# Optimization experiments

Measured on AMD Instinct MI355X. Metric: run time of the kernel, lower is better.

Reference implementation:

```python
import jax, jax.numpy as jnp
import numpy as np

B, S, E, H = 8, 2048, 512, 8
HD = E // H
N_IND = 64


def setup_inputs() -> dict:
    key = jax.random.key(0)
    ks = jax.random.split(key, 10)
    s = 1.0 / np.sqrt(E)
    return {
        "x": jax.random.normal(ks[0], (B, S, E), jnp.float32),
        "Wq": jax.random.normal(ks[1], (E, E), jnp.float32) * s,
        "bq": jax.random.normal(ks[2], (E,), jnp.float32) * s,
        "Wk": jax.random.normal(ks[3], (E, E), jnp.float32) * s,
        "bk": jax.random.normal(ks[4], (E,), jnp.float32) * s,
        "Wv": jax.random.normal(ks[5], (E, E), jnp.float32) * s,
        "bv": jax.random.normal(ks[6], (E,), jnp.float32) * s,
        "Wo": jax.random.normal(ks[7], (E, E), jnp.float32) * s,
        "bo": jax.random.normal(ks[8], (E,), jnp.float32) * s,
        "industry_ids": jax.random.randint(ks[9], (S,), 0, N_IND, jnp.int32),
    }


def reference(x, Wq, bq, Wk, bk, Wv, bv, Wo, bo, industry_ids):
    # same-industry block mask [S, S]; every row attends at least to itself
    mask = industry_ids[:, None] == industry_ids[None, :]
    # projections (torch Linear: y = x @ W.T + b)
    q = (x @ Wq.T + bq).reshape(B, S, H, HD).transpose(0, 2, 1, 3)  # [B,H,S,HD]
    k = (x @ Wk.T + bk).reshape(B, S, H, HD).transpose(0, 2, 1, 3)
    v = (x @ Wv.T + bv).reshape(B, S, H, HD).transpose(0, 2, 1, 3)
    scores = jnp.einsum("bhqd,bhkd->bhqk", q, k) / np.sqrt(HD).astype(jnp.float32)
    scores = jnp.where(mask[None, None, :, :], scores, -jnp.inf)
    attn = jax.nn.softmax(scores, axis=-1)  # dropout is identity at inference
    out = jnp.einsum("bhqk,bhkd->bhqd", attn, v)
    out = out.transpose(0, 2, 1, 3).reshape(B, S, E)
    return out @ Wo.T + bo
```

## Files before the change

kernel.cpp:

```cpp
#include <hip/hip_runtime.h>
#include <cstdint>

#define DEVFN __device__ __forceinline__

typedef __bf16 bf16x8 __attribute__((ext_vector_type(8)));
typedef float f32x4 __attribute__((ext_vector_type(4)));
typedef unsigned int uint;

constexpr int Bc = 8, Sc = 2048, Ec = 512, Hc = 8, HDc = 64, NI = 64;
constexpr int Mtot = Bc * Sc;
constexpr int Kdim = Ec;
constexpr int MAXITEMS = 128;

DEVFN unsigned short f2bf(float f) {
  unsigned u = __builtin_bit_cast(unsigned, f);
  u += 0x7fffu + ((u >> 16) & 1u);
  return (unsigned short)(u >> 16);
}

typedef const void __attribute__((address_space(1))) gvoid_t;
typedef void __attribute__((address_space(3))) lvoid_t;
DEVFN void gload16(const void* g, void* l) {
  __builtin_amdgcn_global_load_lds((gvoid_t*)g, (lvoid_t*)l, 16, 0, 0);
}

DEVFN uint cvtpk(float lo, float hi) {
  uint r;
  asm("v_cvt_pk_bf16_f32 %0, %1, %2" : "=v"(r) : "v"(lo), "v"(hi));
  return r;
}

#define WAIT_VM_BARRIER(N)                                            \
  do {                                                                \
    asm volatile("s_waitcnt vmcnt(" #N ")\n\ts_barrier" ::: "memory"); \
    __builtin_amdgcn_sched_barrier(0);                                \
  } while (0)
#define WAIT_LGKM_BARRIER()                                            \
  do {                                                                 \
    asm volatile("s_waitcnt lgkmcnt(0)\n\ts_barrier" ::: "memory");    \
    __builtin_amdgcn_sched_barrier(0);                                 \
  } while (0)

__global__ void prep2_kernel(const int* __restrict__ ids, int* __restrict__ perm,
                             int* __restrict__ gstart, int* __restrict__ gsz,
                             int* __restrict__ items, int* __restrict__ nitems,
                             const float* __restrict__ Wq, const float* __restrict__ Wk,
                             const float* __restrict__ Wv, const float* __restrict__ Wo,
                             ushort* __restrict__ Wcat, ushort* __restrict__ Wob,
                             const float* __restrict__ x, ushort* __restrict__ xb) {
  if (blockIdx.x == 0) {
    __shared__ int sid[Sc];
    __shared__ int hist[NI];
    __shared__ int base[NI];
    int t = threadIdx.x;
    if (t < NI) hist[t] = 0;
    for (int i = t; i < Sc; i += 256) sid[i] = ids[i];
    __syncthreads();
    for (int i = t; i < Sc; i += 256) atomicAdd(&hist[sid[i]], 1);
    __syncthreads();
    if (t == 0) {
      int run = 0;
      for (int g = 0; g < NI; ++g) { base[g] = run; run += hist[g]; }
      int cnt = 0;
      for (int g = 0; g < NI; ++g)
        for (int q0 = 0; q0 < hist[g]; q0 += 32) items[cnt++] = (g << 16) | q0;
      *nitems = cnt;
    }
    __syncthreads();
    if (t < NI) { gstart[t] = base[t]; gsz[t] = hist[t]; }
    int lane = t & 63, w = t >> 6;
    for (int g = w; g < NI; g += 4) {
      int run = base[g];
      for (int c = 0; c < Sc; c += 64) {
        int tok = c + lane;
        int id = sid[tok];
        unsigned long long mask = __ballot(id == g);
        if (id == g) {
          int rank = __popcll(mask & ((1ull << lane) - 1ull));
          perm[run + rank] = tok;
        }
        run += __popcll(mask);
      }
    }
  } else if (blockIdx.x <= 1024) {
    int i = (blockIdx.x - 1) * 256 + threadIdx.x;
    int idx = i * 4;
    int n = idx >> 9, k = idx & 511;
    const float* src;
    ushort* dst;
    if (n < 512)       { src = Wq + (size_t)n * 512 + k;          dst = Wcat + (size_t)n * 512 + k; }
    else if (n < 1024) { src = Wk + (size_t)(n - 512) * 512 + k;  dst = Wcat + (size_t)n * 512 + k; }
    else if (n < 1536) { src = Wv + (size_t)(n - 1024) * 512 + k; dst = Wcat + (size_t)n * 512 + k; }
    else               { src = Wo + (size_t)(n - 1536) * 512 + k; dst = Wob + (size_t)(n - 1536) * 512 + k; }
    float4 v = *(const float4*)src;
    ushort4 o = {f2bf(v.x), f2bf(v.y), f2bf(v.z), f2bf(v.w)};
    *(ushort4*)dst = o;
  } else {
    int i = (blockIdx.x - 1025) * 256 + threadIdx.x;
    float4 v = ((const float4*)x)[i];
    ushort4 o = {f2bf(v.x), f2bf(v.y), f2bf(v.z), f2bf(v.w)};
    ((ushort4*)xb)[i] = o;
  }
}

__global__ __launch_bounds__(256) void gemm_qkv128(
    const ushort* __restrict__ A, const ushort* __restrict__ Bw,
    const float* __restrict__ bias0, const float* __restrict__ bias1,
    const float* __restrict__ bias2, const int* __restrict__ permarg,
    ushort* __restrict__ qkvout) {
  constexpr int NK = Kdim / 64;
  __shared__ __align__(16) char ldsraw[65536];
  ushort* sAb = (ushort*)ldsraw;
  ushort* sBb = (ushort*)(ldsraw + 32768);
  const int tid = threadIdx.x;
  const int lane = tid & 63;
  const int wave = tid >> 6;
  const int wr = wave >> 1, wc = wave & 1;
  const int orig = blockIdx.x;
  const int xcd = orig & 7, gl = orig >> 3;
  const int mbase = (xcd * 16 + (gl & 15)) * 128;
  const int nbase = (gl >> 4) * 128;

  f32x4 acc[4][4] = {};

  const int rowS = wave * 32 + (lane >> 3);
  const int kc = lane & 7;
  const int mb_hi = mbase & ~(Sc - 1);

  int arow[4];
#pragma unroll
  for (int c = 0; c < 4; ++c)
    arow[c] = mb_hi | permarg[(mbase + rowS + c * 8) & (Sc - 1)];

  auto stage = [&](int buf, int kt) {
    const int k0 = kt * 64;
#pragma unroll
    for (int c = 0; c < 4; ++c) {
      int row = rowS + c * 8;
      int kcp = (kc ^ (row & 7)) * 8;
      gload16(A + (size_t)arow[c] * Kdim + k0 + kcp,
              sAb + buf * 8192 + (wave * 256 + c * 64) * 8);
      gload16(Bw + (size_t)(nbase + row) * Kdim + k0 + kcp,
              sBb + buf * 8192 + (wave * 256 + c * 64) * 8);
    }
  };

  stage(0, 0);
  stage(1, 1);

  for (int kt = 0; kt < NK; ++kt) {
    const int cur = kt & 1;
    if (kt < NK - 1) {
      WAIT_VM_BARRIER(8);
    } else {
      WAIT_VM_BARRIER(0);
    }

    const char* Ab = (const char*)(sAb + cur * 8192);
    const char* Bb = (const char*)(sBb + cur * 8192);
    __builtin_amdgcn_s_setprio(1);
#pragma unroll
    for (int kk = 0; kk < 2; ++kk) {
      bf16x8 af[4], bfv[4];
#pragma unroll
      for (int i = 0; i < 4; ++i) {
        int row = wr * 64 + i * 16 + (lane & 15);
        int off = row * 128 + kk * 64 + (lane >> 4) * 16;
        off ^= (row & 7) << 4;
        af[i] = *(const bf16x8*)(Ab + off);
      }
#pragma unroll
      for (int j = 0; j < 4; ++j) {
        int col = wc * 64 + j * 16 + (lane & 15);
        int off = col * 128 + kk * 64 + (lane >> 4) * 16;
        off ^= (col & 7) << 4;
        bfv[j] = *(const bf16x8*)(Bb + off);
      }
#pragma unroll
      for (int i = 0; i < 4; ++i)
#pragma unroll
        for (int j = 0; j < 4; ++j)
          acc[i][j] = __builtin_amdgcn_mfma_f32_16x16x32_bf16(af[i], bfv[j], acc[i][j], 0, 0, 0);
    }
    __builtin_amdgcn_s_setprio(0);

    WAIT_LGKM_BARRIER();
    if (kt + 2 < NK) stage(cur, kt + 2);
  }

  {
    ushort* T = (ushort*)ldsraw;
#pragma unroll
    for (int i = 0; i < 4; ++i) {
#pragma unroll
      for (int j = 0; j < 4; ++j) {
        int nl = wc * 64 + j * 16 + (lane & 15);
        int n = nbase + nl;
        float bv = (n < 512) ? bias0[n] : (n < 1024) ? bias1[n - 512] : bias2[n - 1024];
#pragma unroll
        for (int r = 0; r < 4; ++r) {
          int ml = wr * 64 + i * 16 + (lane >> 4) * 4 + r;
          T[ml * 136 + nl] = f2bf(acc[i][j][r] + bv);
        }
      }
    }
    __syncthreads();
#pragma unroll
    for (int k = 0; k < 8; ++k) {
      int c = tid + 256 * k;
      int row = c >> 4, col8 = (c & 15) * 8;
      uint4 w = *(const uint4*)(T + row * 136 + col8);
      int n0 = nbase + col8;
      int proj = n0 >> 9, h = (n0 >> 6) & 7, d0 = n0 & 63;
      int p = mbase + row;
      int bidx = p >> 11, pl = p & (Sc - 1);
      size_t off = (size_t)proj * ((size_t)Bc * Hc * Sc * HDc) +
                   (size_t)((bidx * Hc + h) * Sc + pl) * HDc + d0;
      *(uint4*)(qkvout + off) = w;
    }
  }
}

__global__ __launch_bounds__(256) void gemm_out128(
    const ushort* __restrict__ A, const ushort* __restrict__ Bw,
    const float* __restrict__ bias0, const int* __restrict__ permarg,
    float* __restrict__ out) {
  constexpr int NK = Kdim / 64;
  constexpr int NTOT = 512;
  __shared__ __align__(16) char ldsraw[65536];
  ushort* sAb = (ushort*)ldsraw;
  ushort* sBb = (ushort*)(ldsraw + 32768);
  const int tid = threadIdx.x;
  const int lane = tid & 63;
  const int wave = tid >> 6;
  const int wr = wave >> 1, wc = wave & 1;
  const int orig = blockIdx.x;
  const int xcd = orig & 7, gl = orig >> 3;
  const int mbase = (xcd * 16 + (gl & 15)) * 128;
  const int nbase = (gl >> 4) * 128;

  f32x4 acc[4][4] = {};

  const int rowS = wave * 32 + (lane >> 3);
  const int kc = lane & 7;

  auto stage = [&](int buf, int kt) {
    const int k0 = kt * 64;
#pragma unroll
    for (int c = 0; c < 4; ++c) {
      int row = rowS + c * 8;
      int kcp = (kc ^ (row & 7)) * 8;
      gload16(A + (size_t)(mbase + row) * Kdim + k0 + kcp,
              sAb + buf * 8192 + (wave * 256 + c * 64) * 8);
      gload16(Bw + (size_t)(nbase + row) * Kdim + k0 + kcp,
              sBb + buf * 8192 + (wave * 256 + c * 64) * 8);
    }
  };

  stage(0, 0);
  stage(1, 1);

  for (int kt = 0; kt < NK; ++kt) {
    const int cur = kt & 1;
    if (kt < NK - 1) {
      WAIT_VM_BARRIER(8);
    } else {
      WAIT_VM_BARRIER(0);
    }

    const char* Ab = (const char*)(sAb + cur * 8192);
    const char* Bb = (const char*)(sBb + cur * 8192);
    __builtin_amdgcn_s_setprio(1);
#pragma unroll
    for (int kk = 0; kk < 2; ++kk) {
      bf16x8 af[4], bfv[4];
#pragma unroll
      for (int i = 0; i < 4; ++i) {
        int row = wr * 64 + i * 16 + (lane & 15);
        int off = row * 128 + kk * 64 + (lane >> 4) * 16;
        off ^= (row & 7) << 4;
        af[i] = *(const bf16x8*)(Ab + off);
      }
#pragma unroll
      for (int j = 0; j < 4; ++j) {
        int col = wc * 64 + j * 16 + (lane & 15);
        int off = col * 128 + kk * 64 + (lane >> 4) * 16;
        off ^= (col & 7) << 4;
        bfv[j] = *(const bf16x8*)(Bb + off);
      }
#pragma unroll
      for (int i = 0; i < 4; ++i)
#pragma unroll
        for (int j = 0; j < 4; ++j)
          acc[i][j] = __builtin_amdgcn_mfma_f32_16x16x32_bf16(af[i], bfv[j], acc[i][j], 0, 0, 0);
    }
    __builtin_amdgcn_s_setprio(0);

    WAIT_LGKM_BARRIER();
    if (kt + 2 < NK) stage(cur, kt + 2);
  }

  float* T = (float*)ldsraw;
#pragma unroll
  for (int i = 0; i < 4; ++i) {
#pragma unroll
    for (int j = 0; j < 4; ++j) {
      int nl = wc * 64 + j * 16 + (lane & 15);
      float bv = bias0[nbase + nl];
#pragma unroll
      for (int r = 0; r < 4; ++r) {
        int ml = wr * 64 + i * 16 + (lane >> 4) * 4 + r;
        T[ml * 128 + nl] = acc[i][j][r] + bv;
      }
    }
  }
  __syncthreads();
#pragma unroll
  for (int k = 0; k < 16; ++k) {
    int c = tid + 256 * k;
    int row = c >> 5, col4 = (c & 31) * 4;
    float4 w = *(const float4*)(T + row * 128 + col4);
    int p = mbase + row;
    int bidx = p >> 11;
    int orow = (bidx << 11) | permarg[p & (Sc - 1)];
    *(float4*)(out + (size_t)orow * NTOT + nbase + col4) = w;
  }
}

__global__ __launch_bounds__(64) void attn5_kernel(
    const ushort* __restrict__ qkv, const int* __restrict__ gstart,
    const int* __restrict__ gsz, const int* __restrict__ items,
    const int* __restrict__ nitems, ushort* __restrict__ obuf) {
  __shared__ __align__(16) ushort vt[64 * 40];
  if ((int)blockIdx.x >= *nitems) return;
  const int iv = items[blockIdx.x];
  const int g = iv >> 16, q0 = iv & 0xffff;
  const int bh = blockIdx.y;
  const int start = gstart[g], n = gsz[g];
  const int lane = threadIdx.x;
  const int ql = lane & 15, lg = lane >> 4;

  const size_t planeSz = (size_t)Bc * Hc * Sc * HDc;
  const ushort* qb = qkv + (size_t)bh * Sc * HDc;
  const ushort* kb = qb + planeSz;
  const ushort* vb = kb + planeSz;

  bf16x8 qf[2][2];
#pragma unroll
  for (int qt = 0; qt < 2; ++qt) {
    int row = min(start + q0 + qt * 16 + ql, Sc - 1);
#pragma unroll
    for (int h = 0; h < 2; ++h)
      qf[qt][h] = *(const bf16x8*)(qb + (size_t)row * HDc + h * 32 + lg * 8);
  }

  f32x4 oacc[2][4] = {};
  float lsum[2] = {0.f, 0.f};

  const int vk = lane & 31;
  const int vh = (lane >> 5) * 32;
  const int Lbase = 4 * (ql + 32 * (lg & 1));

  const int npair = (n + 31) >> 5;
  for (int pr = 0; pr < npair; ++pr) {
    const int c0 = pr * 32;
    int vrow = min(start + c0 + vk, Sc - 1);
    const uint4* vp = (const uint4*)(vb + (size_t)vrow * HDc + vh);
    uint4 v0 = vp[0], v1 = vp[1], v2 = vp[2], v3 = vp[3];

    bf16x8 kf[2][2];
#pragma unroll
    for (int t = 0; t < 2; ++t) {
      int row = min(start + c0 + t * 16 + ql, Sc - 1);
#pragma unroll
      for (int h = 0; h < 2; ++h)
        kf[t][h] = *(const bf16x8*)(kb + (size_t)row * HDc + h * 32 + lg * 8);
    }

    uint pw[2][4];
#pragma unroll
    for (int qt = 0; qt < 2; ++qt) {
      f32x4 s0 = {}, s1 = {};
      s0 = __builtin_amdgcn_mfma_f32_16x16x32_bf16(kf[0][0], qf[qt][0], s0, 0, 0, 0);
      s0 = __builtin_amdgcn_mfma_f32_16x16x32_bf16(kf[0][1], qf[qt][1], s0, 0, 0, 0);
      s1 = __builtin_amdgcn_mfma_f32_16x16x32_bf16(kf[1][0], qf[qt][0], s1, 0, 0, 0);
      s1 = __builtin_amdgcn_mfma_f32_16x16x32_bf16(kf[1][1], qf[qt][1], s1, 0, 0, 0);
      float p0[4], p1[4];
      float ls = 0.f;
#pragma unroll
      for (int r = 0; r < 4; ++r) {
        int kk = c0 + 4 * lg + r;
        float e0 = (kk < n) ? __expf(s0[r] * 0.125f) : 0.f;
        float e1 = (kk + 16 < n) ? __expf(s1[r] * 0.125f) : 0.f;
        p0[r] = e0;
        p1[r] = e1;
        ls += e0 + e1;
      }
      lsum[qt] += ls;
      uint a0 = cvtpk(p0[0], p0[1]), b0 = cvtpk(p0[2], p0[3]);
      uint a1 = cvtpk(p1[0], p1[1]), b1 = cvtpk(p1[2], p1[3]);
      uint pA0 = __builtin_amdgcn_ds_bpermute(Lbase, a0);
      uint pB0 = __builtin_amdgcn_ds_bpermute(Lbase, b0);
      uint pA1 = __builtin_amdgcn_ds_bpermute(Lbase, a1);
      uint pB1 = __builtin_amdgcn_ds_bpermute(Lbase, b1);
      uint pC0 = __builtin_amdgcn_ds_bpermute(Lbase + 64, a0);
      uint pD0 = __builtin_amdgcn_ds_bpermute(Lbase + 64, b0);
      uint pC1 = __builtin_amdgcn_ds_bpermute(Lbase + 64, a1);
      uint pD1 = __builtin_amdgcn_ds_bpermute(Lbase + 64, b1);
      bool t0 = lg < 2;
      pw[qt][0] = t0 ? pA0 : pA1;
      pw[qt][1] = t0 ? pB0 : pB1;
      pw[qt][2] = t0 ? pC0 : pC1;
      pw[qt][3] = t0 ? pD0 : pD1;
    }

    {
      uint w[16] = {v0.x, v0.y, v0.z, v0.w, v1.x, v1.y, v1.z, v1.w,
                    v2.x, v2.y, v2.z, v2.w, v3.x, v3.y, v3.z, v3.w};
#pragma unroll
      for (int i = 0; i < 16; ++i) {
        vt[(vh + 2 * i) * 40 + vk] = (ushort)(w[i] & 0xffffu);
        vt[(vh + 2 * i + 1) * 40 + vk] = (ushort)(w[i] >> 16);
      }
    }
    asm volatile("s_waitcnt lgkmcnt(0)" ::: "memory");
    __builtin_amdgcn_sched_barrier(0);
    bf16x8 vf[4];
#pragma unroll
    for (int dq = 0; dq < 4; ++dq)
      vf[dq] = *(const bf16x8*)(vt + (dq * 16 + ql) * 40 + lg * 8);
    asm volatile("s_waitcnt lgkmcnt(0)" ::: "memory");
    __builtin_amdgcn_sched_barrier(0);
#pragma unroll
    for (int qt = 0; qt < 2; ++qt) {
      union { uint u[4]; bf16x8 v; } pf;
      pf.u[0] = pw[qt][0]; pf.u[1] = pw[qt][1]; pf.u[2] = pw[qt][2]; pf.u[3] = pw[qt][3];
#pragma unroll
      for (int dq = 0; dq < 4; ++dq)
        oacc[qt][dq] = __builtin_amdgcn_mfma_f32_16x16x32_bf16(vf[dq], pf.v, oacc[qt][dq], 0, 0, 0);
    }
  }

#pragma unroll
  for (int qt = 0; qt < 2; ++qt) {
    float l = lsum[qt];
    l += __shfl_xor(l, 16);
    l += __shfl_xor(l, 32);
    float inv = 1.f / l;
    int qi = q0 + qt * 16 + ql;
    if (qi < n) {
      int p = start + qi;
      ushort* op = obuf + (size_t)((bh >> 3) * Sc + p) * Ec + (bh & 7) * HDc + lg * 4;
#pragma unroll
      for (int dq = 0; dq < 4; ++dq) {
        uint w0 = cvtpk(oacc[qt][dq][0] * inv, oacc[qt][dq][1] * inv);
        uint w1 = cvtpk(oacc[qt][dq][2] * inv, oacc[qt][dq][3] * inv);
        uint2 wv = {w0, w1};
        *(uint2*)(op + dq * 16) = wv;
      }
    }
  }
}

extern "C" void kernel_launch(void* const* d_in, const int* in_sizes, int n_in,
                              void* d_out, int out_size, void* d_ws, size_t ws_size,
                              hipStream_t stream) {
  const float* x  = (const float*)d_in[0];
  const float* Wq = (const float*)d_in[1];
  const float* bq = (const float*)d_in[2];
  const float* Wk = (const float*)d_in[3];
  const float* bk = (const float*)d_in[4];
  const float* Wv = (const float*)d_in[5];
  const float* bv = (const float*)d_in[6];
  const float* Wo = (const float*)d_in[7];
  const float* bo = (const float*)d_in[8];
  const int* ids  = (const int*)d_in[9];
  float* out = (float*)d_out;

  char* ws = (char*)d_ws;
  ushort* xb   = (ushort*)(ws);
  ushort* Wcat = (ushort*)(ws + 16777216);
  ushort* Wob  = (ushort*)(ws + 18350080);
  ushort* qkv  = (ushort*)(ws + 18874368);
  ushort* obuf = (ushort*)(ws + 69206016);
  int* perm    = (int*)(ws + 85983232);
  int* gstart  = perm + Sc;
  int* gsz     = gstart + NI;
  int* items   = gsz + NI;
  int* nitems  = items + MAXITEMS;

  prep2_kernel<<<dim3(1 + 1024 + Mtot * Ec / 4 / 256), dim3(256), 0, stream>>>(
      ids, perm, gstart, gsz, items, nitems, Wq, Wk, Wv, Wo, Wcat, Wob, x, xb);
  gemm_qkv128<<<dim3(Mtot / 128 * 12), dim3(256), 0, stream>>>(xb, Wcat, bq, bk, bv, perm, qkv);
  attn5_kernel<<<dim3(MAXITEMS, Bc * Hc), dim3(64), 0, stream>>>(qkv, gstart, gsz, items,
                                                                 nitems, obuf);
  gemm_out128<<<dim3(Mtot / 128 * 4), dim3(256), 0, stream>>>(obuf, Wob, bo, perm, out);
}
```

Baseline: 118.4 us.

## Fuse all stages into one persistent kernel with grid-wide barriers

Replaces the four separate launches (prep, QKV GEMM, attention, output GEMM) with one persistent 512-block kernel that loops over work units and separates stages with atomic-counter grid barriers. The goal is to remove launch overhead and inter-kernel drain gaps. In exchange, each stage now runs on a fixed 512-block grid with strided work loops, capped at 2 blocks per CU, and attention runs four waves per block instead of one-wave blocks. The spin barriers require every block to be co-resident, and an extra memset launch is added to reset the counters.

```diff
diff --git a/kernel.cpp b/kernel.cpp
--- a/kernel.cpp
+++ b/kernel.cpp
@@ -11,6 +11,7 @@
 constexpr int Mtot = Bc * Sc;
 constexpr int Kdim = Ec;
 constexpr int MAXITEMS = 128;
+constexpr int NBLK = 512;
 
 DEVFN unsigned short f2bf(float f) {
   unsigned u = __builtin_bit_cast(unsigned, f);
@@ -41,18 +42,38 @@
     __builtin_amdgcn_sched_barrier(0);                                 \
   } while (0)
 
-__global__ void prep2_kernel(const int* __restrict__ ids, int* __restrict__ perm,
-                             int* __restrict__ gstart, int* __restrict__ gsz,
-                             int* __restrict__ items, int* __restrict__ nitems,
-                             const float* __restrict__ Wq, const float* __restrict__ Wk,
-                             const float* __restrict__ Wv, const float* __restrict__ Wo,
-                             ushort* __restrict__ Wcat, ushort* __restrict__ Wob,
-                             const float* __restrict__ x, ushort* __restrict__ xb) {
+DEVFN void grid_bar(int* cnt) {
+  __syncthreads();
+  if (threadIdx.x == 0) {
+    __threadfence();
+    atomicAdd(cnt, 1);
+    while (atomicAdd(cnt, 0) < NBLK) __builtin_amdgcn_s_sleep(2);
+    __threadfence();
+  }
+  __syncthreads();
+}
+
+__global__ __launch_bounds__(256, 2) void mega_kernel(
+    const int* __restrict__ ids, const float* __restrict__ x,
+    const float* __restrict__ Wq, const float* __restrict__ Wk,
+    const float* __restrict__ Wv, const float* __restrict__ Wo,
+    const float* __restrict__ bq, const float* __restrict__ bk,
+    const float* __restrict__ bv, const float* __restrict__ bo,
+    ushort* __restrict__ xb, ushort* __restrict__ Wcat, ushort* __restrict__ Wob,
+    ushort* __restrict__ qkv, ushort* __restrict__ obuf,
+    int* __restrict__ perm, int* __restrict__ gstart, int* __restrict__ gsz,
+    int* __restrict__ items, int* __restrict__ nitems,
+    float* __restrict__ out, int* __restrict__ bars) {
+  __shared__ __align__(16) char ldsraw[65536];
+  const int tid = threadIdx.x;
+  const int lane = tid & 63;
+  const int wave = tid >> 6;
+
   if (blockIdx.x == 0) {
-    __shared__ int sid[Sc];
-    __shared__ int hist[NI];
-    __shared__ int base[NI];
-    int t = threadIdx.x;
+    int* sid = (int*)ldsraw;
+    int* hist = sid + Sc;
+    int* base = hist + NI;
+    int t = tid;
     if (t < NI) hist[t] = 0;
     for (int i = t; i < Sc; i += 256) sid[i] = ids[i];
     __syncthreads();
@@ -68,7 +89,7 @@
     }
     __syncthreads();
     if (t < NI) { gstart[t] = base[t]; gsz[t] = hist[t]; }
-    int lane = t & 63, w = t >> 6;
+    int w = t >> 6;
     for (int g = w; g < NI; g += 4) {
       int run = base[g];
       for (int c = 0; c < Sc; c += 64) {
@@ -82,382 +103,363 @@
         run += __popcll(mask);
       }
     }
-  } else if (blockIdx.x <= 1024) {
-    int i = (blockIdx.x - 1) * 256 + threadIdx.x;
-    int idx = i * 4;
-    int n = idx >> 9, k = idx & 511;
-    const float* src;
-    ushort* dst;
-    if (n < 512)       { src = Wq + (size_t)n * 512 + k;          dst = Wcat + (size_t)n * 512 + k; }
-    else if (n < 1024) { src = Wk + (size_t)(n - 512) * 512 + k;  dst = Wcat + (size_t)n * 512 + k; }
-    else if (n < 1536) { src = Wv + (size_t)(n - 1024) * 512 + k; dst = Wcat + (size_t)n * 512 + k; }
-    else               { src = Wo + (size_t)(n - 1536) * 512 + k; dst = Wob + (size_t)(n - 1536) * 512 + k; }
-    float4 v = *(const float4*)src;
-    ushort4 o = {f2bf(v.x), f2bf(v.y), f2bf(v.z), f2bf(v.w)};
-    *(ushort4*)dst = o;
   } else {
-    int i = (blockIdx.x - 1025) * 256 + threadIdx.x;
-    float4 v = ((const float4*)x)[i];
-    ushort4 o = {f2bf(v.x), f2bf(v.y), f2bf(v.z), f2bf(v.w)};
-    ((ushort4*)xb)[i] = o;
+#pragma unroll 1
+    for (int k = 0; k < 19; ++k) {
+      int unit = (blockIdx.x - 1) + 511 * k;
+      if (unit >= 9216) break;
+      if (unit < 1024) {
+        int i = unit * 256 + tid;
+        int idx = i * 4;
+        int n = idx >> 9, kk = idx & 511;
+        const float* src;
+        ushort* dst;
+        if (n < 512)       { src = Wq + (size_t)n * 512 + kk;          dst = Wcat + (size_t)n * 512 + kk; }
+        else if (n < 1024) { src = Wk + (size_t)(n - 512) * 512 + kk;  dst = Wcat + (size_t)n * 512 + kk; }
+        else if (n < 1536) { src = Wv + (size_t)(n - 1024) * 512 + kk; dst = Wcat + (size_t)n * 512 + kk; }
+        else               { src = Wo + (size_t)(n - 1536) * 512 + kk; dst = Wob + (size_t)(n - 1536) * 512 + kk; }
+        float4 v = *(const float4*)src;
+        ushort4 o = {f2bf(v.x), f2bf(v.y), f2bf(v.z), f2bf(v.w)};
+        *(ushort4*)dst = o;
+      } else {
+        int i = (unit - 1024) * 256 + tid;
+        float4 v = ((const float4*)x)[i];
+        ushort4 o = {f2bf(v.x), f2bf(v.y), f2bf(v.z), f2bf(v.w)};
+        ((ushort4*)xb)[i] = o;
+      }
+    }
   }
-}
-
-__global__ __launch_bounds__(256) void gemm_qkv128(
-    const ushort* __restrict__ A, const ushort* __restrict__ Bw,
-    const float* __restrict__ bias0, const float* __restrict__ bias1,
-    const float* __restrict__ bias2, const int* __restrict__ permarg,
-    ushort* __restrict__ qkvout) {
-  constexpr int NK = Kdim / 64;
-  __shared__ __align__(16) char ldsraw[65536];
-  ushort* sAb = (ushort*)ldsraw;
-  ushort* sBb = (ushort*)(ldsraw + 32768);
-  const int tid = threadIdx.x;
-  const int lane = tid & 63;
-  const int wave = tid >> 6;
-  const int wr = wave >> 1, wc = wave & 1;
-  const int orig = blockIdx.x;
-  const int xcd = orig & 7, gl = orig >> 3;
-  const int mbase = (xcd * 16 + (gl & 15)) * 128;
-  const int nbase = (gl >> 4) * 128;
-
-  f32x4 acc[4][4] = {};
-
-  const int rowS = wave * 32 + (lane >> 3);
-  const int kc = lane & 7;
-  const int mb_hi = mbase & ~(Sc - 1);
-
-  int arow[4];
-#pragma unroll
-  for (int c = 0; c < 4; ++c)
-    arow[c] = mb_hi | permarg[(mbase + rowS + c * 8) & (Sc - 1)];
-
-  auto stage = [&](int buf, int kt) {
-    const int k0 = kt * 64;
-#pragma unroll
-    for (int c = 0; c < 4; ++c) {
-      int row = rowS + c * 8;
-      int kcp = (kc ^ (row & 7)) * 8;
-      gload16(A + (size_t)arow[c] * Kdim + k0 + kcp,
-              sAb + buf * 8192 + (wave * 256 + c * 64) * 8);
-      gload16(Bw + (size_t)(nbase + row) * Kdim + k0 + kcp,
-              sBb + buf * 8192 + (wave * 256 + c * 64) * 8);
-    }
-  };
-
-  stage(0, 0);
-  stage(1, 1);
-
-  for (int kt = 0; kt < NK; ++kt) {
-    const int cur = kt & 1;
-    if (kt < NK - 1) {
-      WAIT_VM_BARRIER(8);
-    } else {
-      WAIT_VM_BARRIER(0);
-    }
-
-    const char* Ab = (const char*)(sAb + cur * 8192);
-    const char* Bb = (const char*)(sBb + cur * 8192);
-    __builtin_amdgcn_s_setprio(1);
-#pragma unroll
-    for (int kk = 0; kk < 2; ++kk) {
-      bf16x8 af[4], bfv[4];
-#pragma unroll
-      for (int i = 0; i < 4; ++i) {
-        int row = wr * 64 + i * 16 + (lane & 15);
-        int off = row * 128 + kk * 64 + (lane >> 4) * 16;
-        off ^= (row & 7) << 4;
-        af[i] = *(const bf16x8*)(Ab + off);
-      }
-#pragma unroll
-      for (int j = 0; j < 4; ++j) {
-        int col = wc * 64 + j * 16 + (lane & 15);
-        int off = col * 128 + kk * 64 + (lane >> 4) * 16;
-        off ^= (col & 7) << 4;
-        bfv[j] = *(const bf16x8*)(Bb + off);
-      }
-#pragma unroll
-      for (int i = 0; i < 4; ++i)
-#pragma unroll
-        for (int j = 0; j < 4; ++j)
-          acc[i][j] = __builtin_amdgcn_mfma_f32_16x16x32_bf16(af[i], bfv[j], acc[i][j], 0, 0, 0);
-    }
-    __builtin_amdgcn_s_setprio(0);
-
-    WAIT_LGKM_BARRIER();
-    if (kt + 2 < NK) stage(cur, kt + 2);
+  grid_bar(&bars[0]);
+
+  {
+    ushort* sAb = (ushort*)ldsraw;
+    ushort* sBb = (ushort*)(ldsraw + 32768);
+    const int wr = wave >> 1, wc = wave & 1;
+    const int rowS = wave * 32 + (lane >> 3);
+    const int kc = lane & 7;
+    constexpr int NK = Kdim / 64;
+#pragma unroll 1
+    for (int t = blockIdx.x; t < 1536; t += NBLK) {
+      const int xcd = t & 7, gl = t >> 3;
+      const int mbase = (xcd * 16 + (gl & 15)) * 128;
+      const int nbase = (gl >> 4) * 128;
+      const int mb_hi = mbase & ~(Sc - 1);
+      f32x4 acc[4][4] = {};
+      int arow[4];
+#pragma unroll
+      for (int c = 0; c < 4; ++c)
+        arow[c] = mb_hi | perm[(mbase + rowS + c * 8) & (Sc - 1)];
+
+      auto stage = [&](int buf, int kt) {
+        const int k0 = kt * 64;
+#pragma unroll
+        for (int c = 0; c < 4; ++c) {
+          int row = rowS + c * 8;
+          int kcp = (kc ^ (row & 7)) * 8;
+          gload16(xb + (size_t)arow[c] * Kdim + k0 + kcp,
+                  sAb + buf * 8192 + (wave * 256 + c * 64) * 8);
+          gload16(Wcat + (size_t)(nbase + row) * Kdim + k0 + kcp,
+                  sBb + buf * 8192 + (wave * 256 + c * 64) * 8);
+        }
+      };
+
+      stage(0, 0);
+      stage(1, 1);
+      for (int kt = 0; kt < NK; ++kt) {
+        const int cur = kt & 1;
+        if (kt < NK - 1) {
+          WAIT_VM_BARRIER(8);
+        } else {
+          WAIT_VM_BARRIER(0);
+        }
+        const char* Ab = (const char*)(sAb + cur * 8192);
+        const char* Bb = (const char*)(sBb + cur * 8192);
+        __builtin_amdgcn_s_setprio(1);
+#pragma unroll
+        for (int kk = 0; kk < 2; ++kk) {
+          bf16x8 af[4], bfv[4];
+#pragma unroll
+          for (int i = 0; i < 4; ++i) {
+            int row = wr * 64 + i * 16 + (lane & 15);
+            int off = row * 128 + kk * 64 + (lane >> 4) * 16;
+            off ^= (row & 7) << 4;
+            af[i] = *(const bf16x8*)(Ab + off);
+          }
+#pragma unroll
+          for (int j = 0; j < 4; ++j) {
+            int col = wc * 64 + j * 16 + (lane & 15);
+            int off = col * 128 + kk * 64 + (lane >> 4) * 16;
+            off ^= (col & 7) << 4;
+            bfv[j] = *(const bf16x8*)(Bb + off);
+          }
+#pragma unroll
+          for (int i = 0; i < 4; ++i)
+#pragma unroll
+            for (int j = 0; j < 4; ++j)
+              acc[i][j] = __builtin_amdgcn_mfma_f32_16x16x32_bf16(af[i], bfv[j], acc[i][j], 0, 0, 0);
+        }
+        __builtin_amdgcn_s_setprio(0);
+        WAIT_LGKM_BARRIER();
+        if (kt + 2 < NK) stage(cur, kt + 2);
+      }
+
+      {
+        ushort* T = (ushort*)ldsraw;
+#pragma unroll
+        for (int i = 0; i < 4; ++i) {
+#pragma unroll
+          for (int j = 0; j < 4; ++j) {
+            int nl = wc * 64 + j * 16 + (lane & 15);
+            int n = nbase + nl;
+            float bvv = (n < 512) ? bq[n] : (n < 1024) ? bk[n - 512] : bv[n - 1024];
+#pragma unroll
+            for (int r = 0; r < 4; ++r) {
+              int ml = wr * 64 + i * 16 + (lane >> 4) * 4 + r;
+              T[ml * 136 + nl] = f2bf(acc[i][j][r] + bvv);
+            }
+          }
+        }
+        __syncthreads();
+#pragma unroll
+        for (int k = 0; k < 8; ++k) {
+          int c = tid + 256 * k;
+          int row = c >> 4, col8 = (c & 15) * 8;
+          uint4 w = *(const uint4*)(T + row * 136 + col8);
+          int n0 = nbase + col8;
+          int proj = n0 >> 9, h = (n0 >> 6) & 7, d0 = n0 & 63;
+          int p = mbase + row;
+          int bidx = p >> 11, pl = p & (Sc - 1);
+          size_t off = (size_t)proj * ((size_t)Bc * Hc * Sc * HDc) +
+                       (size_t)((bidx * Hc + h) * Sc + pl) * HDc + d0;
+          *(uint4*)(qkv + off) = w;
+        }
+      }
+      __syncthreads();
+    }
   }
+  grid_bar(&bars[1]);
 
   {
-    ushort* T = (ushort*)ldsraw;
+    const int NIT = *nitems;
+    ushort* vt = (ushort*)(ldsraw + wave * 5120);
+    const int ql = lane & 15, lg = lane >> 4;
+    const size_t planeSz = (size_t)Bc * Hc * Sc * HDc;
+    const int vk = lane & 31;
+    const int vh = (lane >> 5) * 32;
+    const int Lbase = 4 * (ql + 32 * (lg & 1));
+#pragma unroll 1
+    for (int k = 0; k < 4; ++k) {
+      const int u = (blockIdx.x * 4 + wave) + 2048 * k;
+      const int item = u & (MAXITEMS - 1);
+      const int bh = u >> 7;
+      if (item >= NIT) continue;
+      const int iv = items[item];
+      const int g = iv >> 16, q0 = iv & 0xffff;
+      const int start = gstart[g], n = gsz[g];
+      const ushort* qb = qkv + (size_t)bh * Sc * HDc;
+      const ushort* kb = qb + planeSz;
+      const ushort* vb = kb + planeSz;
+
+      bf16x8 qf[2][2];
+#pragma unroll
+      for (int qt = 0; qt < 2; ++qt) {
+        int row = min(start + q0 + qt * 16 + ql, Sc - 1);
+#pragma unroll
+        for (int h = 0; h < 2; ++h)
+          qf[qt][h] = *(const bf16x8*)(qb + (size_t)row * HDc + h * 32 + lg * 8);
+      }
+      f32x4 oacc[2][4] = {};
+      float lsum[2] = {0.f, 0.f};
+      const int npair = (n + 31) >> 5;
+      for (int pr = 0; pr < npair; ++pr) {
+        const int c0 = pr * 32;
+        int vrow = min(start + c0 + vk, Sc - 1);
+        const uint4* vp = (const uint4*)(vb + (size_t)vrow * HDc + vh);
+        uint4 v0 = vp[0], v1 = vp[1], v2 = vp[2], v3 = vp[3];
+        bf16x8 kf[2][2];
+#pragma unroll
+        for (int t2 = 0; t2 < 2; ++t2) {
+          int row = min(start + c0 + t2 * 16 + ql, Sc - 1);
+#pragma unroll
+          for (int h = 0; h < 2; ++h)
+            kf[t2][h] = *(const bf16x8*)(kb + (size_t)row * HDc + h * 32 + lg * 8);
+        }
+        uint pw[2][4];
+#pragma unroll
+        for (int qt = 0; qt < 2; ++qt) {
+          f32x4 s0 = {}, s1 = {};
+          s0 = __builtin_amdgcn_mfma_f32_16x16x32_bf16(kf[0][0], qf[qt][0], s0, 0, 0, 0);
+          s0 = __builtin_amdgcn_mfma_f32_16x16x32_bf16(kf[0][1], qf[qt][1], s0, 0, 0, 0);
+          s1 = __builtin_amdgcn_mfma_f32_16x16x32_bf16(kf[1][0], qf[qt][0], s1, 0, 0, 0);
+          s1 = __builtin_amdgcn_mfma_f32_16x16x32_bf16(kf[1][1], qf[qt][1], s1, 0, 0, 0);
+          float p0[4], p1[4];
+          float ls = 0.f;
+#pragma unroll
+          for (int r = 0; r < 4; ++r) {
+            int kk = c0 + 4 * lg + r;
+            float e0 = (kk < n) ? __expf(s0[r] * 0.125f) : 0.f;
+            float e1 = (kk + 16 < n) ? __expf(s1[r] * 0.125f) : 0.f;
+            p0[r] = e0;
+            p1[r] = e1;
+            ls += e0 + e1;
+          }
+          lsum[qt] += ls;
+          uint a0 = cvtpk(p0[0], p0[1]), b0 = cvtpk(p0[2], p0[3]);
+          uint a1 = cvtpk(p1[0], p1[1]), b1 = cvtpk(p1[2], p1[3]);
+          uint pA0 = __builtin_amdgcn_ds_bpermute(Lbase, a0);
+          uint pB0 = __builtin_amdgcn_ds_bpermute(Lbase, b0);
+          uint pA1 = __builtin_amdgcn_ds_bpermute(Lbase, a1);
+          uint pB1 = __builtin_amdgcn_ds_bpermute(Lbase, b1);
+          uint pC0 = __builtin_amdgcn_ds_bpermute(Lbase + 64, a0);
+          uint pD0 = __builtin_amdgcn_ds_bpermute(Lbase + 64, b0);
+          uint pC1 = __builtin_amdgcn_ds_bpermute(Lbase + 64, a1);
+          uint pD1 = __builtin_amdgcn_ds_bpermute(Lbase + 64, b1);
+          bool t0 = lg < 2;
+          pw[qt][0] = t0 ? pA0 : pA1;
+          pw[qt][1] = t0 ? pB0 : pB1;
+          pw[qt][2] = t0 ? pC0 : pC1;
+          pw[qt][3] = t0 ? pD0 : pD1;
+        }
+        {
+          uint w[16] = {v0.x, v0.y, v0.z, v0.w, v1.x, v1.y, v1.z, v1.w,
+                        v2.x, v2.y, v2.z, v2.w, v3.x, v3.y, v3.z, v3.w};
+#pragma unroll
+          for (int i = 0; i < 16; ++i) {
+            vt[(vh + 2 * i) * 40 + vk] = (ushort)(w[i] & 0xffffu);
+            vt[(vh + 2 * i + 1) * 40 + vk] = (ushort)(w[i] >> 16);
+          }
+        }
+        asm volatile("s_waitcnt lgkmcnt(0)" ::: "memory");
+        __builtin_amdgcn_sched_barrier(0);
+        bf16x8 vf[4];
+#pragma unroll
+        for (int dq = 0; dq < 4; ++dq)
+          vf[dq] = *(const bf16x8*)(vt + (dq * 16 + ql) * 40 + lg * 8);
+        asm volatile("s_waitcnt lgkmcnt(0)" ::: "memory");
+        __builtin_amdgcn_sched_barrier(0);
+#pragma unroll
+        for (int qt = 0; qt < 2; ++qt) {
+          union { uint u4[4]; bf16x8 v; } pf;
+          pf.u4[0] = pw[qt][0]; pf.u4[1] = pw[qt][1]; pf.u4[2] = pw[qt][2]; pf.u4[3] = pw[qt][3];
+#pragma unroll
+          for (int dq = 0; dq < 4; ++dq)
+            oacc[qt][dq] = __builtin_amdgcn_mfma_f32_16x16x32_bf16(vf[dq], pf.v, oacc[qt][dq], 0, 0, 0);
+        }
+      }
+#pragma unroll
+      for (int qt = 0; qt < 2; ++qt) {
+        float l = lsum[qt];
+        l += __shfl_xor(l, 16);
+        l += __shfl_xor(l, 32);
+        float inv = 1.f / l;
+        int qi = q0 + qt * 16 + ql;
+        if (qi < n) {
+          int p = start + qi;
+          ushort* op = obuf + (size_t)((bh >> 3) * Sc + p) * Ec + (bh & 7) * HDc + lg * 4;
+#pragma unroll
+          for (int dq = 0; dq < 4; ++dq) {
+            uint w0 = cvtpk(oacc[qt][dq][0] * inv, oacc[qt][dq][1] * inv);
+            uint w1 = cvtpk(oacc[qt][dq][2] * inv, oacc[qt][dq][3] * inv);
+            uint2 wv2 = {w0, w1};
+            *(uint2*)(op + dq * 16) = wv2;
+          }
+        }
+      }
+    }
+  }
+  grid_bar(&bars[2]);
+
+  {
+    constexpr int NK = Kdim / 64;
+    constexpr int NTOT = 512;
+    ushort* sAb = (ushort*)ldsraw;
+    ushort* sBb = (ushort*)(ldsraw + 32768);
+    const int wr = wave >> 1, wc = wave & 1;
+    const int t = blockIdx.x;
+    const int xcd = t & 7, gl = t >> 3;
+    const int mbase = (xcd * 16 + (gl & 15)) * 128;
+    const int nbase = (gl >> 4) * 128;
+    f32x4 acc[4][4] = {};
+    const int rowS = wave * 32 + (lane >> 3);
+    const int kc = lane & 7;
+
+    auto stage = [&](int buf, int kt) {
+      const int k0 = kt * 64;
+#pragma unroll
+      for (int c = 0; c < 4; ++c) {
+        int row = rowS + c * 8;
+        int kcp = (kc ^ (row & 7)) * 8;
+        gload16(obuf + (size_t)(mbase + row) * Kdim + k0 + kcp,
+                sAb + buf * 8192 + (wave * 256 + c * 64) * 8);
+        gload16(Wob + (size_t)(nbase + row) * Kdim + k0 + kcp,
+                sBb + buf * 8192 + (wave * 256 + c * 64) * 8);
+      }
+    };
+
+    stage(0, 0);
+    stage(1, 1);
+    for (int kt = 0; kt < NK; ++kt) {
+      const int cur = kt & 1;
+      if (kt < NK - 1) {
+        WAIT_VM_BARRIER(8);
+      } else {
+        WAIT_VM_BARRIER(0);
+      }
+      const char* Ab = (const char*)(sAb + cur * 8192);
+      const char* Bb = (const char*)(sBb + cur * 8192);
+      __builtin_amdgcn_s_setprio(1);
+#pragma unroll
+      for (int kk = 0; kk < 2; ++kk) {
+        bf16x8 af[4], bfv[4];
+#pragma unroll
+        for (int i = 0; i < 4; ++i) {
+          int row = wr * 64 + i * 16 + (lane & 15);
+          int off = row * 128 + kk * 64 + (lane >> 4) * 16;
+          off ^= (row & 7) << 4;
+          af[i] = *(const bf16x8*)(Ab + off);
+        }
+#pragma unroll
+        for (int j = 0; j < 4; ++j) {
+          int col = wc * 64 + j * 16 + (lane & 15);
+          int off = col * 128 + kk * 64 + (lane >> 4) * 16;
+          off ^= (col & 7) << 4;
+          bfv[j] = *(const bf16x8*)(Bb + off);
+        }
+#pragma unroll
+        for (int i = 0; i < 4; ++i)
+#pragma unroll
+          for (int j = 0; j < 4; ++j)
+            acc[i][j] = __builtin_amdgcn_mfma_f32_16x16x32_bf16(af[i], bfv[j], acc[i][j], 0, 0, 0);
+      }
+      __builtin_amdgcn_s_setprio(0);
+      WAIT_LGKM_BARRIER();
+      if (kt + 2 < NK) stage(cur, kt + 2);
+    }
+
+    float* T = (float*)ldsraw;
 #pragma unroll
     for (int i = 0; i < 4; ++i) {
 #pragma unroll
       for (int j = 0; j < 4; ++j) {
         int nl = wc * 64 + j * 16 + (lane & 15);
-        int n = nbase + nl;
-        float bv = (n < 512) ? bias0[n] : (n < 1024) ? bias1[n - 512] : bias2[n - 1024];
+        float bvv = bo[nbase + nl];
 #pragma unroll
         for (int r = 0; r < 4; ++r) {
           int ml = wr * 64 + i * 16 + (lane >> 4) * 4 + r;
-          T[ml * 136 + nl] = f2bf(acc[i][j][r] + bv);
+          T[ml * 128 + nl] = acc[i][j][r] + bvv;
         }
       }
     }
     __syncthreads();
 #pragma unroll
-    for (int k = 0; k < 8; ++k) {
+    for (int k = 0; k < 16; ++k) {
       int c = tid + 256 * k;
-      int row = c >> 4, col8 = (c & 15) * 8;
-      uint4 w = *(const uint4*)(T + row * 136 + col8);
-      int n0 = nbase + col8;
-      int proj = n0 >> 9, h = (n0 >> 6) & 7, d0 = n0 & 63;
+      int row = c >> 5, col4 = (c & 31) * 4;
+      float4 w = *(const float4*)(T + row * 128 + col4);
       int p = mbase + row;
-      int bidx = p >> 11, pl = p & (Sc - 1);
-      size_t off = (size_t)proj * ((size_t)Bc * Hc * Sc * HDc) +
-                   (size_t)((bidx * Hc + h) * Sc + pl) * HDc + d0;
-      *(uint4*)(qkvout + off) = w;
-    }
-  }
-}
-
-__global__ __launch_bounds__(256) void gemm_out128(
-    const ushort* __restrict__ A, const ushort* __restrict__ Bw,
-    const float* __restrict__ bias0, const int* __restrict__ permarg,
-    float* __restrict__ out) {
-  constexpr int NK = Kdim / 64;
-  constexpr int NTOT = 512;
-  __shared__ __align__(16) char ldsraw[65536];
-  ushort* sAb = (ushort*)ldsraw;
-  ushort* sBb = (ushort*)(ldsraw + 32768);
-  const int tid = threadIdx.x;
-  const int lane = tid & 63;
-  const int wave = tid >> 6;
-  const int wr = wave >> 1, wc = wave & 1;
-  const int orig = blockIdx.x;
-  const int xcd = orig & 7, gl = orig >> 3;
-  const int mbase = (xcd * 16 + (gl & 15)) * 128;
-  const int nbase = (gl >> 4) * 128;
-
-  f32x4 acc[4][4] = {};
-
-  const int rowS = wave * 32 + (lane >> 3);
-  const int kc = lane & 7;
-
-  auto stage = [&](int buf, int kt) {
-    const int k0 = kt * 64;
-#pragma unroll
-    for (int c = 0; c < 4; ++c) {
-      int row = rowS + c * 8;
-      int kcp = (kc ^ (row & 7)) * 8;
-      gload16(A + (size_t)(mbase + row) * Kdim + k0 + kcp,
-              sAb + buf * 8192 + (wave * 256 + c * 64) * 8);
-      gload16(Bw + (size_t)(nbase + row) * Kdim + k0 + kcp,
-              sBb + buf * 8192 + (wave * 256 + c * 64) * 8);
-    }
-  };
-
-  stage(0, 0);
-  stage(1, 1);
-
-  for (int kt = 0; kt < NK; ++kt) {
-    const int cur = kt & 1;
-    if (kt < NK - 1) {
-      WAIT_VM_BARRIER(8);
-    } else {
-      WAIT_VM_BARRIER(0);
-    }
-
-    const char* Ab = (const char*)(sAb + cur * 8192);
-    const char* Bb = (const char*)(sBb + cur * 8192);
-    __builtin_amdgcn_s_setprio(1);
-#pragma unroll
-    for (int kk = 0; kk < 2; ++kk) {
-      bf16x8 af[4], bfv[4];
-#pragma unroll
-      for (int i = 0; i < 4; ++i) {
-        int row = wr * 64 + i * 16 + (lane & 15);
-        int off = row * 128 + kk * 64 + (lane >> 4) * 16;
-        off ^= (row & 7) << 4;
-        af[i] = *(const bf16x8*)(Ab + off);
-      }
-#pragma unroll
-      for (int j = 0; j < 4; ++j) {
-        int col = wc * 64 + j * 16 + (lane & 15);
-        int off = col * 128 + kk * 64 + (lane >> 4) * 16;
-        off ^= (col & 7) << 4;
-        bfv[j] = *(const bf16x8*)(Bb + off);
-      }
-#pragma unroll
-      for (int i = 0; i < 4; ++i)
-#pragma unroll
-        for (int j = 0; j < 4; ++j)
-          acc[i][j] = __builtin_amdgcn_mfma_f32_16x16x32_bf16(af[i], bfv[j], acc[i][j], 0, 0, 0);
-    }
-    __builtin_amdgcn_s_setprio(0);
-
-    WAIT_LGKM_BARRIER();
-    if (kt + 2 < NK) stage(cur, kt + 2);
-  }
-
-  float* T = (float*)ldsraw;
-#pragma unroll
-  for (int i = 0; i < 4; ++i) {
-#pragma unroll
-    for (int j = 0; j < 4; ++j) {
-      int nl = wc * 64 + j * 16 + (lane & 15);
-      float bv = bias0[nbase + nl];
-#pragma unroll
-      for (int r = 0; r < 4; ++r) {
-        int ml = wr * 64 + i * 16 + (lane >> 4) * 4 + r;
-        T[ml * 128 + nl] = acc[i][j][r] + bv;
-      }
-    }
-  }
-  __syncthreads();
-#pragma unroll
-  for (int k = 0; k < 16; ++k) {
-    int c = tid + 256 * k;
-    int row = c >> 5, col4 = (c & 31) * 4;
-    float4 w = *(const float4*)(T + row * 128 + col4);
-    int p = mbase + row;
-    int bidx = p >> 11;
-    int orow = (bidx << 11) | permarg[p & (Sc - 1)];
-    *(float4*)(out + (size_t)orow * NTOT + nbase + col4) = w;
-  }
-}
-
-__global__ __launch_bounds__(64) void attn5_kernel(
-    const ushort* __restrict__ qkv, const int* __restrict__ gstart,
-    const int* __restrict__ gsz, const int* __restrict__ items,
-    const int* __restrict__ nitems, ushort* __restrict__ obuf) {
-  __shared__ __align__(16) ushort vt[64 * 40];
-  if ((int)blockIdx.x >= *nitems) return;
-  const int iv = items[blockIdx.x];
-  const int g = iv >> 16, q0 = iv & 0xffff;
-  const int bh = blockIdx.y;
-  const int start = gstart[g], n = gsz[g];
-  const int lane = threadIdx.x;
-  const int ql = lane & 15, lg = lane >> 4;
-
-  const size_t planeSz = (size_t)Bc * Hc * Sc * HDc;
-  const ushort* qb = qkv + (size_t)bh * Sc * HDc;
-  const ushort* kb = qb + planeSz;
-  const ushort* vb = kb + planeSz;
-
-  bf16x8 qf[2][2];
-#pragma unroll
-  for (int qt = 0; qt < 2; ++qt) {
-    int row = min(start + q0 + qt * 16 + ql, Sc - 1);
-#pragma unroll
-    for (int h = 0; h < 2; ++h)
-      qf[qt][h] = *(const bf16x8*)(qb + (size_t)row * HDc + h * 32 + lg * 8);
-  }
-
-  f32x4 oacc[2][4] = {};
-  float lsum[2] = {0.f, 0.f};
-
-  const int vk = lane & 31;
-  const int vh = (lane >> 5) * 32;
-  const int Lbase = 4 * (ql + 32 * (lg & 1));
-
-  const int npair = (n + 31) >> 5;
-  for (int pr = 0; pr < npair; ++pr) {
-    const int c0 = pr * 32;
-    int vrow = min(start + c0 + vk, Sc - 1);
-    const uint4* vp = (const uint4*)(vb + (size_t)vrow * HDc + vh);
-    uint4 v0 = vp[0], v1 = vp[1], v2 = vp[2], v3 = vp[3];
-
-    bf16x8 kf[2][2];
-#pragma unroll
-    for (int t = 0; t < 2; ++t) {
-      int row = min(start + c0 + t * 16 + ql, Sc - 1);
-#pragma unroll
-      for (int h = 0; h < 2; ++h)
-        kf[t][h] = *(const bf16x8*)(kb + (size_t)row * HDc + h * 32 + lg * 8);
-    }
-
-    uint pw[2][4];
-#pragma unroll
-    for (int qt = 0; qt < 2; ++qt) {
-      f32x4 s0 = {}, s1 = {};
-      s0 = __builtin_amdgcn_mfma_f32_16x16x32_bf16(kf[0][0], qf[qt][0], s0, 0, 0, 0);
-      s0 = __builtin_amdgcn_mfma_f32_16x16x32_bf16(kf[0][1], qf[qt][1], s0, 0, 0, 0);
-      s1 = __builtin_amdgcn_mfma_f32_16x16x32_bf16(kf[1][0], qf[qt][0], s1, 0, 0, 0);
-      s1 = __builtin_amdgcn_mfma_f32_16x16x32_bf16(kf[1][1], qf[qt][1], s1, 0, 0, 0);
-      float p0[4], p1[4];
-      float ls = 0.f;
-#pragma unroll
-      for (int r = 0; r < 4; ++r) {
-        int kk = c0 + 4 * lg + r;
-        float e0 = (kk < n) ? __expf(s0[r] * 0.125f) : 0.f;
-        float e1 = (kk + 16 < n) ? __expf(s1[r] * 0.125f) : 0.f;
-        p0[r] = e0;
-        p1[r] = e1;
-        ls += e0 + e1;
-      }
-      lsum[qt] += ls;
-      uint a0 = cvtpk(p0[0], p0[1]), b0 = cvtpk(p0[2], p0[3]);
-      uint a1 = cvtpk(p1[0], p1[1]), b1 = cvtpk(p1[2], p1[3]);
-      uint pA0 = __builtin_amdgcn_ds_bpermute(Lbase, a0);
-      uint pB0 = __builtin_amdgcn_ds_bpermute(Lbase, b0);
-      uint pA1 = __builtin_amdgcn_ds_bpermute(Lbase, a1);
-      uint pB1 = __builtin_amdgcn_ds_bpermute(Lbase, b1);
-      uint pC0 = __builtin_amdgcn_ds_bpermute(Lbase + 64, a0);
-      uint pD0 = __builtin_amdgcn_ds_bpermute(Lbase + 64, b0);
-      uint pC1 = __builtin_amdgcn_ds_bpermute(Lbase + 64, a1);
-      uint pD1 = __builtin_amdgcn_ds_bpermute(Lbase + 64, b1);
-      bool t0 = lg < 2;
-      pw[qt][0] = t0 ? pA0 : pA1;
-      pw[qt][1] = t0 ? pB0 : pB1;
-      pw[qt][2] = t0 ? pC0 : pC1;
-      pw[qt][3] = t0 ? pD0 : pD1;
-    }
-
-    {
-      uint w[16] = {v0.x, v0.y, v0.z, v0.w, v1.x, v1.y, v1.z, v1.w,
-                    v2.x, v2.y, v2.z, v2.w, v3.x, v3.y, v3.z, v3.w};
-#pragma unroll
-      for (int i = 0; i < 16; ++i) {
-        vt[(vh + 2 * i) * 40 + vk] = (ushort)(w[i] & 0xffffu);
-        vt[(vh + 2 * i + 1) * 40 + vk] = (ushort)(w[i] >> 16);
-      }
-    }
-    asm volatile("s_waitcnt lgkmcnt(0)" ::: "memory");
-    __builtin_amdgcn_sched_barrier(0);
-    bf16x8 vf[4];
-#pragma unroll
-    for (int dq = 0; dq < 4; ++dq)
-      vf[dq] = *(const bf16x8*)(vt + (dq * 16 + ql) * 40 + lg * 8);
-    asm volatile("s_waitcnt lgkmcnt(0)" ::: "memory");
-    __builtin_amdgcn_sched_barrier(0);
-#pragma unroll
-    for (int qt = 0; qt < 2; ++qt) {
-      union { uint u[4]; bf16x8 v; } pf;
-      pf.u[0] = pw[qt][0]; pf.u[1] = pw[qt][1]; pf.u[2] = pw[qt][2]; pf.u[3] = pw[qt][3];
-#pragma unroll
-      for (int dq = 0; dq < 4; ++dq)
-        oacc[qt][dq] = __builtin_amdgcn_mfma_f32_16x16x32_bf16(vf[dq], pf.v, oacc[qt][dq], 0, 0, 0);
-    }
-  }
-
-#pragma unroll
-  for (int qt = 0; qt < 2; ++qt) {
-    float l = lsum[qt];
-    l += __shfl_xor(l, 16);
-    l += __shfl_xor(l, 32);
-    float inv = 1.f / l;
-    int qi = q0 + qt * 16 + ql;
-    if (qi < n) {
-      int p = start + qi;
-      ushort* op = obuf + (size_t)((bh >> 3) * Sc + p) * Ec + (bh & 7) * HDc + lg * 4;
-#pragma unroll
-      for (int dq = 0; dq < 4; ++dq) {
-        uint w0 = cvtpk(oacc[qt][dq][0] * inv, oacc[qt][dq][1] * inv);
-        uint w1 = cvtpk(oacc[qt][dq][2] * inv, oacc[qt][dq][3] * inv);
-        uint2 wv = {w0, w1};
-        *(uint2*)(op + dq * 16) = wv;
-      }
+      int bidx = p >> 11;
+      int orow = (bidx << 11) | perm[p & (Sc - 1)];
+      *(float4*)(out + (size_t)orow * NTOT + nbase + col4) = w;
     }
   }
 }
@@ -488,11 +490,10 @@
   int* gsz     = gstart + NI;
   int* items   = gsz + NI;
   int* nitems  = items + MAXITEMS;
-
-  prep2_kernel<<<dim3(1 + 1024 + Mtot * Ec / 4 / 256), dim3(256), 0, stream>>>(
-      ids, perm, gstart, gsz, items, nitems, Wq, Wk, Wv, Wo, Wcat, Wob, x, xb);
-  gemm_qkv128<<<dim3(Mtot / 128 * 12), dim3(256), 0, stream>>>(xb, Wcat, bq, bk, bv, perm, qkv);
-  attn5_kernel<<<dim3(MAXITEMS, Bc * Hc), dim3(64), 0, stream>>>(qkv, gstart, gsz, items,
-                                                                 nitems, obuf);
-  gemm_out128<<<dim3(Mtot / 128 * 4), dim3(256), 0, stream>>>(obuf, Wob, bo, perm, out);
-}
+  int* bars    = nitems + 1;
+
+  (void)hipMemsetAsync(bars, 0, 3 * sizeof(int), stream);
+  mega_kernel<<<dim3(NBLK), dim3(256), 0, stream>>>(
+      ids, x, Wq, Wk, Wv, Wo, bq, bk, bv, bo, xb, Wcat, Wob, qkv, obuf,
+      perm, gstart, gsz, items, nitems, out, bars);
+}
```

Result: slower. 268.0 us (+126.3%).
